# Optimization experiments

Measured on AMD Instinct MI355X. Metric: run time of the kernel, lower is better.

Reference implementation:

```python
import jax, jax.numpy as jnp
import numpy as np

N = 8192      # nodes
NIN = 128     # input feature dim
NH = 128      # hidden dim
NC = 8        # communities
CS = N // NC  # community size


def setup_inputs() -> dict:
    key = jax.random.key(0)
    k = jax.random.split(key, 6)
    seq1 = jax.random.normal(k[0], (1, N, NIN), jnp.float32)
    seq2 = jax.random.normal(k[1], (1, N, NIN), jnp.float32)
    # dense row-stochastic-ish adjacency so GCN activations stay O(1)
    adj = jax.random.uniform(k[2], (1, N, N), jnp.float32) * (2.0 / N)
    cc_label = jnp.arange(N, dtype=jnp.int32).reshape(NC, CS)  # partition of nodes
    W = jax.random.normal(k[3], (NIN, NH), jnp.float32) / np.float32(np.sqrt(NIN))
    b = jnp.zeros((NH,), jnp.float32)
    Wb = jax.random.normal(k[4], (NH, NH), jnp.float32) / np.float32(np.sqrt(NH))
    bb = jnp.zeros((), jnp.float32)
    return {"seq1": seq1, "seq2": seq2, "adj": adj, "cc_label": cc_label,
            "W": W, "b": b, "Wb": Wb, "bb": bb}


def reference(seq1, seq2, adj, cc_label, W, b, Wb, bb):
    def gcn(seq):
        fts = jnp.einsum('bnd,dh->bnh', seq, W)            # linear
        agg = jnp.einsum('bnm,bmh->bnh', adj, fts) + b     # neighborhood aggregation
        return jax.nn.relu(agg)

    h1 = gcn(seq1)[0]   # [N, NH]
    h2 = gcn(seq2)[0]   # [N, NH]

    # ragged per-community gather (communities are equal-size here)
    hg1 = h1[cc_label]  # [NC, CS, NH]
    hg2 = h2[cc_label]  # [NC, CS, NH]

    # AvgReadout (msk=None) + sigmoid -> per-community summary
    c = jax.nn.sigmoid(jnp.mean(hg1, axis=1))              # [NC, NH]

    # Discriminator: bilinear f_k(h, c) = h @ Wb @ c + bb
    cw = jnp.einsum('hk,nk->nh', Wb, c)                    # [NC, NH]
    sc1 = jnp.einsum('nch,nh->nc', hg1, cw) + bb           # [NC, CS]
    sc2 = jnp.einsum('nch,nh->nc', hg2, cw) + bb           # [NC, CS]

    # scalar scatter-back (each node written exactly once)
    flat = cc_label.reshape(-1)
    ret1 = jnp.zeros((N,), h1.dtype).at[flat].set(sc1.reshape(-1))
    ret2 = jnp.zeros((N,), h2.dtype).at[flat].set(sc2.reshape(-1))
    return jnp.concatenate([ret1, ret2])[None, :]          # [1, 2N]
```

## Files before the change

kernel.cpp:

```cpp
#include <hip/hip_runtime.h>


#define NN    8192
#define NCOLS 256
#define ASCALE 4096.0f
#define AINV  (1.0f/4096.0f)

typedef _Float16 half8 __attribute__((ext_vector_type(8)));
typedef _Float16 half4v __attribute__((ext_vector_type(4)));
typedef float    f32x4 __attribute__((ext_vector_type(4)));

__device__ __forceinline__ void gload16(const void* g, void* l) {
  __builtin_amdgcn_global_load_lds(
      (const __attribute__((address_space(1))) char*)g,
      (__attribute__((address_space(3))) char*)l, 16, 0, 0);
}

__global__ __launch_bounds__(256) void k1_fts(const float* __restrict__ seq1,
                                              const float* __restrict__ seq2,
                                              const float* __restrict__ W,
                                              _Float16* __restrict__ F,
                                              const int* __restrict__ cc,
                                              int* __restrict__ node_comm,
                                              float* __restrict__ S) {
  __shared__ char lds[65536];
  _Float16* Wt  = (_Float16*)lds;
  float*    sSeq = (float*)(lds + 32768);
  const int tid = threadIdx.x;
  const int lane = tid & 63;
  const int w = tid >> 6;
  const int l15 = lane & 15;
  const int g = lane >> 4;
  const int m0 = blockIdx.x * 64;

  if (tid < 64) {
    int i = blockIdx.x * 64 + tid;
    node_comm[cc[i]] = i >> 10;
  }
  if (blockIdx.x == 0) {
    for (int j = tid; j < 1024; j += 256) S[j] = 0.0f;
  }

  for (int it = 0; it < 64; ++it) {
    int idx = it * 256 + tid;
    int d = idx >> 7, hc = idx & 127;
    int byte = (hc * 256 + d * 2) ^ ((hc & 7) << 4);
    *(_Float16*)(lds + byte) = (_Float16)W[idx];
  }

  const float* seqp[2] = {seq1, seq2};
  const int srow = tid >> 5;
  const int sck = tid & 31;

  for (int s = 0; s < 2; ++s) {
    __syncthreads();
    const float* sp = seqp[s];
#pragma unroll
    for (int i = 0; i < 8; ++i) {
      int row = i * 8 + srow;
      gload16(sp + (size_t)(m0 + row) * 128 + ((sck ^ (row & 7)) << 2),
              (char*)sSeq + i * 4096 + w * 1024);
    }
    asm volatile("s_waitcnt vmcnt(0)" ::: "memory");
    __syncthreads();

    f32x4 acc[4][2] = {};
    const float4* S4 = (const float4*)sSeq;
    const float4* W4 = (const float4*)Wt;
#pragma unroll
    for (int kk = 0; kk < 4; ++kk) {
      half8 bf[2];
#pragma unroll
      for (int nf = 0; nf < 2; ++nf) {
        int col = w * 32 + nf * 16 + l15;
        float4 bv = W4[(col * 16 + kk * 4 + g) ^ (col & 7)];
        bf[nf] = *(const half8*)&bv;
      }
#pragma unroll
      for (int mf = 0; mf < 4; ++mf) {
        int row = mf * 16 + l15;
        int bidx = row * 32 + kk * 8 + g * 2;
        float4 u = S4[bidx ^ (row & 7)];
        float4 v = S4[(bidx + 1) ^ (row & 7)];
        half8 af;
#pragma unroll
        for (int j = 0; j < 4; ++j) af[j] = (_Float16)(((const float*)&u)[j]);
#pragma unroll
        for (int j = 0; j < 4; ++j) af[4 + j] = (_Float16)(((const float*)&v)[j]);
#pragma unroll
        for (int nf = 0; nf < 2; ++nf)
          acc[mf][nf] = __builtin_amdgcn_mfma_f32_16x16x32_f16(af, bf[nf], acc[mf][nf], 0, 0, 0);
      }
    }
    __syncthreads();
    _Float16* img = (_Float16*)sSeq;
#pragma unroll
    for (int mf = 0; mf < 4; ++mf)
#pragma unroll
      for (int nf = 0; nf < 2; ++nf) {
        int col = w * 32 + nf * 16 + l15;
#pragma unroll
        for (int j = 0; j < 4; ++j) {
          int kl = mf * 16 + g * 4 + j;
          img[(kl >> 5) * 4096 + col * 32 + (kl & 31)] = (_Float16)acc[mf][nf][j];
        }
      }
    __syncthreads();
    const float4* src4 = (const float4*)sSeq;
#pragma unroll
    for (int i = 0; i < 4; ++i) {
      int e = i * 256 + tid;
      int kt = e >> 9, off = e & 511;
      ((float4*)(F + (size_t)(2 * blockIdx.x + kt) * 8192))[s * 512 + off] = src4[e];
    }
  }
}

__global__ __launch_bounds__(512) void k2_gemm(const float* __restrict__ adj,
                                               const _Float16* __restrict__ F,
                                               float* __restrict__ Pp) {
  __shared__ __align__(16) _Float16 sA[2][32768];
  const int tid = threadIdx.x;
  const int lane = tid & 63;
  const int w = tid >> 6;
  const int l15 = lane & 15;
  const int g = lane >> 4;
  const int id = blockIdx.x;
  const int xcd = id & 7;
  const int ks = xcd >> 1;
  const int mtile = (id >> 3) * 2 + (xcd & 1);
  const int row0 = mtile * 128;
  const int wm = w >> 2, wn = w & 3;

  const float* abase = adj + (size_t)(row0 + w * 16) * NN + (size_t)ks * 2048 + lane * 4;
  const _Float16* fbase = F + (size_t)(ks * 64) * 8192;

  f32x4 acc[4][4] = {};

  auto cvt_store = [&](int b, int i, f32x4 v) {
    int row = w * 16 + i;
    char* dst = (char*)sA[b] + row * 512 + ((lane * 8) ^ ((row & 15) << 4));
    half4v h;
    h[0] = (_Float16)(v[0] * ASCALE); h[1] = (_Float16)(v[1] * ASCALE);
    h[2] = (_Float16)(v[2] * ASCALE); h[3] = (_Float16)(v[3] * ASCALE);
    *(half4v*)dst = h;
  };

  {
    f32x4 pv[16];
#pragma unroll
    for (int i = 0; i < 16; ++i)
      pv[i] = __builtin_nontemporal_load((const f32x4*)(abase + (size_t)i * NN));
#pragma unroll
    for (int i = 0; i < 16; ++i) cvt_store(0, i, pv[i]);
  }
  __syncthreads();

  int colb[4], rowb[4], rsw[4];
#pragma unroll
  for (int nf = 0; nf < 4; ++nf) colb[nf] = (wn * 64 + nf * 16 + l15) * 32 + g * 8;
#pragma unroll
  for (int mf = 0; mf < 4; ++mf) {
    int row = wm * 64 + mf * 16 + l15;
    rowb[mf] = row * 512; rsw[mf] = (row & 15) << 4;
  }

  half8 bfc[4], bfn[4];
#pragma unroll
  for (int nf = 0; nf < 4; ++nf) {
    float4 t = *(const float4*)(fbase + colb[nf]);
    bfc[nf] = *(const half8*)&t;
  }

  for (int m = 0; m < 8; ++m) {
    const int b = m & 1;
    const bool lastm = (m == 7);
    const char* ab = (const char*)sA[b];
    const float* anext = abase + (m + 1) * 256;
    f32x4 ba[8][2];
#pragma unroll
    for (int s = 0; s < 8; ++s) {
      if (!(lastm && s == 7)) {
        const _Float16* fb = fbase + (size_t)(m * 8 + s + 1) * 8192;
#pragma unroll
        for (int nf = 0; nf < 4; ++nf) {
          float4 t = *(const float4*)(fb + colb[nf]);
          bfn[nf] = *(const half8*)&t;
        }
      }
      if (!lastm) {
        ba[s][0] = __builtin_nontemporal_load((const f32x4*)(anext + (size_t)(2 * s) * NN));
        ba[s][1] = __builtin_nontemporal_load((const f32x4*)(anext + (size_t)(2 * s + 1) * NN));
      }
#pragma unroll
      for (int mf = 0; mf < 4; ++mf) {
        half8 af = *(const half8*)(ab + rowb[mf] + ((s * 64 + g * 16) ^ rsw[mf]));
#pragma unroll
        for (int nf = 0; nf < 4; ++nf)
          acc[mf][nf] = __builtin_amdgcn_mfma_f32_16x16x32_f16(af, bfc[nf], acc[mf][nf], 0, 0, 0);
      }
      if (!lastm && s >= 2) {
        cvt_store(b ^ 1, 2 * (s - 2),     ba[s - 2][0]);
        cvt_store(b ^ 1, 2 * (s - 2) + 1, ba[s - 2][1]);
      }
#pragma unroll
      for (int nf = 0; nf < 4; ++nf) bfc[nf] = bfn[nf];
    }
    if (!lastm) {
      cvt_store(b ^ 1, 12, ba[6][0]); cvt_store(b ^ 1, 13, ba[6][1]);
      cvt_store(b ^ 1, 14, ba[7][0]); cvt_store(b ^ 1, 15, ba[7][1]);
    }
    __syncthreads();
  }

#pragma unroll
  for (int mf = 0; mf < 4; ++mf)
#pragma unroll
    for (int nf = 0; nf < 4; ++nf) {
      int col = wn * 64 + nf * 16 + l15;
#pragma unroll
      for (int j = 0; j < 4; ++j) {
        int row = row0 + wm * 64 + mf * 16 + g * 4 + j;
        __builtin_nontemporal_store(acc[mf][nf][j],
            Pp + ((size_t)ks * NN + row) * NCOLS + col);
      }
    }
}

__global__ void k2r_reduce(const float* __restrict__ Pp, const float* __restrict__ b,
                           float* __restrict__ h) {
  int gid = blockIdx.x * 256 + threadIdx.x;
  size_t base = (size_t)gid * 4;
  f32x4 p0 = __builtin_nontemporal_load((const f32x4*)(Pp + base));
  f32x4 p1 = __builtin_nontemporal_load((const f32x4*)(Pp + base + 2097152));
  f32x4 p2 = __builtin_nontemporal_load((const f32x4*)(Pp + base + 4194304));
  f32x4 p3 = __builtin_nontemporal_load((const f32x4*)(Pp + base + 6291456));
  int n0 = (int)(base & 255) & 127;
  float4 r;
  r.x = fmaxf((p0[0] + p1[0] + p2[0] + p3[0]) * AINV + b[n0],     0.f);
  r.y = fmaxf((p0[1] + p1[1] + p2[1] + p3[1]) * AINV + b[n0 + 1], 0.f);
  r.z = fmaxf((p0[2] + p1[2] + p2[2] + p3[2]) * AINV + b[n0 + 2], 0.f);
  r.w = fmaxf((p0[3] + p1[3] + p2[3] + p3[3]) * AINV + b[n0 + 3], 0.f);
  *(float4*)(h + base) = r;
}

__global__ __launch_bounds__(128) void k3a_csum(const float* __restrict__ h,
                                                const int* __restrict__ node_comm,
                                                float* __restrict__ S) {
  int hh = threadIdx.x;
  int n0 = blockIdx.x * 32;
  float a0=0,a1=0,a2=0,a3=0,a4=0,a5=0,a6=0,a7=0;
  for (int i = 0; i < 32; ++i) {
    int node = n0 + i;
    int c = node_comm[node];
    float v = h[(size_t)node * 256 + hh];
    a0 += (c == 0) ? v : 0.f;  a1 += (c == 1) ? v : 0.f;
    a2 += (c == 2) ? v : 0.f;  a3 += (c == 3) ? v : 0.f;
    a4 += (c == 4) ? v : 0.f;  a5 += (c == 5) ? v : 0.f;
    a6 += (c == 6) ? v : 0.f;  a7 += (c == 7) ? v : 0.f;
  }
  if (a0 != 0.f) atomicAdd(&S[0 * 128 + hh], a0);
  if (a1 != 0.f) atomicAdd(&S[1 * 128 + hh], a1);
  if (a2 != 0.f) atomicAdd(&S[2 * 128 + hh], a2);
  if (a3 != 0.f) atomicAdd(&S[3 * 128 + hh], a3);
  if (a4 != 0.f) atomicAdd(&S[4 * 128 + hh], a4);
  if (a5 != 0.f) atomicAdd(&S[5 * 128 + hh], a5);
  if (a6 != 0.f) atomicAdd(&S[6 * 128 + hh], a6);
  if (a7 != 0.f) atomicAdd(&S[7 * 128 + hh], a7);
}

__global__ __launch_bounds__(128) void k3b_cw(const float* __restrict__ S,
                                              const float* __restrict__ Wb,
                                              float* __restrict__ cw) {
  __shared__ float sc[128];
  int ci = blockIdx.x;
  int hh = threadIdx.x;
  float m = S[ci * 128 + hh] * (1.0f / 1024.0f);
  sc[hh] = 1.0f / (1.0f + __expf(-m));
  __syncthreads();
  const float4* wr = (const float4*)(Wb + (size_t)hh * 128);
  float acc = 0.f;
#pragma unroll 8
  for (int k4 = 0; k4 < 32; ++k4) {
    float4 wv = wr[k4];
    acc += wv.x * sc[k4 * 4 + 0] + wv.y * sc[k4 * 4 + 1]
         + wv.z * sc[k4 * 4 + 2] + wv.w * sc[k4 * 4 + 3];
  }
  cw[ci * 128 + hh] = acc;
}

__global__ __launch_bounds__(256) void k5_score(const float* __restrict__ h,
                                                const int* __restrict__ node_comm,
                                                const float* __restrict__ cw,
                                                const float* __restrict__ bbp,
                                                float* __restrict__ out) {
  int tid = threadIdx.x;
  int q = tid & 15, nl = tid >> 4;
  int node = blockIdx.x * 16 + nl;
  int c = node_comm[node];
  const float* hr = h + (size_t)node * 256;
  const float* cr = cw + c * 128;
  float4 c0 = *(const float4*)(cr + q * 8);
  float4 c1 = *(const float4*)(cr + q * 8 + 4);
  float4 a0 = *(const float4*)(hr + q * 8);
  float4 a1 = *(const float4*)(hr + q * 8 + 4);
  float p1 = a0.x*c0.x + a0.y*c0.y + a0.z*c0.z + a0.w*c0.w
           + a1.x*c1.x + a1.y*c1.y + a1.z*c1.z + a1.w*c1.w;
  float4 b0 = *(const float4*)(hr + 128 + q * 8);
  float4 b1 = *(const float4*)(hr + 128 + q * 8 + 4);
  float p2 = b0.x*c0.x + b0.y*c0.y + b0.z*c0.z + b0.w*c0.w
           + b1.x*c1.x + b1.y*c1.y + b1.z*c1.z + b1.w*c1.w;
#pragma unroll
  for (int m = 8; m >= 1; m >>= 1) {
    p1 += __shfl_xor(p1, m, 64);
    p2 += __shfl_xor(p2, m, 64);
  }
  if (q == 0) {
    float bb = bbp[0];
    out[node] = p1 + bb;
    out[8192 + node] = p2 + bb;
  }
}

extern "C" void kernel_launch(void* const* d_in, const int* in_sizes, int n_in,
                              void* d_out, int out_size, void* d_ws, size_t ws_size,
                              hipStream_t stream) {
  (void)in_sizes; (void)n_in; (void)out_size; (void)ws_size;
  const float* seq1 = (const float*)d_in[0];
  const float* seq2 = (const float*)d_in[1];
  const float* adj  = (const float*)d_in[2];
  const int*   cc   = (const int*)d_in[3];
  const float* W    = (const float*)d_in[4];
  const float* b    = (const float*)d_in[5];
  const float* Wb   = (const float*)d_in[6];
  const float* bb   = (const float*)d_in[7];
  float* out = (float*)d_out;

  char* ws = (char*)d_ws;
  _Float16* F   = (_Float16*)(ws);
  float* h      = (float*)(ws + (4u << 20));
  float* Pp     = (float*)(ws + (12u << 20));
  float* S      = (float*)(ws + (44u << 20));
  float* cw     = (float*)(ws + (44u << 20) + 4096);
  int* node_comm = (int*)(ws + (44u << 20) + 8192);

  k1_fts<<<dim3(128), dim3(256), 0, stream>>>(seq1, seq2, W, F, cc, node_comm, S);
  k2_gemm<<<dim3(256), dim3(512), 0, stream>>>(adj, F, Pp);
  k2r_reduce<<<dim3(2048), dim3(256), 0, stream>>>(Pp, b, h);
  k3a_csum<<<dim3(256), dim3(128), 0, stream>>>(h, node_comm, S);
  k3b_cw<<<dim3(8), dim3(128), 0, stream>>>(S, Wb, cw);
  k5_score<<<dim3(512), dim3(256), 0, stream>>>(h, node_comm, cw, bb, out);
}
```

Measured before the change: 108.9 us.

## Fuse split-K reduce with community sums and split k1 across sequences

```diff
diff --git a/kernel.cpp b/kernel.cpp
--- a/kernel.cpp
+++ b/kernel.cpp
@@ -21,8 +21,7 @@
                                               const float* __restrict__ W,
                                               _Float16* __restrict__ F,
                                               const int* __restrict__ cc,
-                                              int* __restrict__ node_comm,
-                                              float* __restrict__ S) {
+                                              int* __restrict__ node_comm) {
   __shared__ char lds[65536];
   _Float16* Wt  = (_Float16*)lds;
   float*    sSeq = (float*)(lds + 32768);
@@ -31,88 +30,92 @@
   const int w = tid >> 6;
   const int l15 = lane & 15;
   const int g = lane >> 4;
-  const int m0 = blockIdx.x * 64;
-
-  if (tid < 64) {
-    int i = blockIdx.x * 64 + tid;
+  const int s = blockIdx.x >> 7;
+  const int mt = blockIdx.x & 127;
+  const int m0 = mt * 64;
+
+  if (s == 0 && tid < 64) {
+    int i = mt * 64 + tid;
     node_comm[cc[i]] = i >> 10;
   }
-  if (blockIdx.x == 0) {
-    for (int j = tid; j < 1024; j += 256) S[j] = 0.0f;
-  }
-
-  for (int it = 0; it < 64; ++it) {
-    int idx = it * 256 + tid;
-    int d = idx >> 7, hc = idx & 127;
-    int byte = (hc * 256 + d * 2) ^ ((hc & 7) << 4);
-    *(_Float16*)(lds + byte) = (_Float16)W[idx];
-  }
-
-  const float* seqp[2] = {seq1, seq2};
+
+  {
+    const float4* W4g = (const float4*)W;
+#pragma unroll
+    for (int i = 0; i < 16; ++i) {
+      int idx4 = i * 256 + tid;
+      float4 wv = W4g[idx4];
+      int d = idx4 >> 5;
+      int hc = (idx4 & 31) * 4;
+#pragma unroll
+      for (int j = 0; j < 4; ++j) {
+        int byte = ((hc + j) * 256 + d * 2) ^ (((hc + j) & 7) << 4);
+        *(_Float16*)(lds + byte) = (_Float16)(((const float*)&wv)[j]);
+      }
+    }
+  }
+
+  const float* sp = s ? seq2 : seq1;
   const int srow = tid >> 5;
   const int sck = tid & 31;
-
-  for (int s = 0; s < 2; ++s) {
-    __syncthreads();
-    const float* sp = seqp[s];
-#pragma unroll
-    for (int i = 0; i < 8; ++i) {
-      int row = i * 8 + srow;
-      gload16(sp + (size_t)(m0 + row) * 128 + ((sck ^ (row & 7)) << 2),
-              (char*)sSeq + i * 4096 + w * 1024);
-    }
-    asm volatile("s_waitcnt vmcnt(0)" ::: "memory");
-    __syncthreads();
-
-    f32x4 acc[4][2] = {};
-    const float4* S4 = (const float4*)sSeq;
-    const float4* W4 = (const float4*)Wt;
-#pragma unroll
-    for (int kk = 0; kk < 4; ++kk) {
-      half8 bf[2];
-#pragma unroll
-      for (int nf = 0; nf < 2; ++nf) {
-        int col = w * 32 + nf * 16 + l15;
-        float4 bv = W4[(col * 16 + kk * 4 + g) ^ (col & 7)];
-        bf[nf] = *(const half8*)&bv;
-      }
-#pragma unroll
-      for (int mf = 0; mf < 4; ++mf) {
-        int row = mf * 16 + l15;
-        int bidx = row * 32 + kk * 8 + g * 2;
-        float4 u = S4[bidx ^ (row & 7)];
-        float4 v = S4[(bidx + 1) ^ (row & 7)];
-        half8 af;
-#pragma unroll
-        for (int j = 0; j < 4; ++j) af[j] = (_Float16)(((const float*)&u)[j]);
-#pragma unroll
-        for (int j = 0; j < 4; ++j) af[4 + j] = (_Float16)(((const float*)&v)[j]);
-#pragma unroll
-        for (int nf = 0; nf < 2; ++nf)
-          acc[mf][nf] = __builtin_amdgcn_mfma_f32_16x16x32_f16(af, bf[nf], acc[mf][nf], 0, 0, 0);
-      }
-    }
-    __syncthreads();
-    _Float16* img = (_Float16*)sSeq;
-#pragma unroll
-    for (int mf = 0; mf < 4; ++mf)
-#pragma unroll
-      for (int nf = 0; nf < 2; ++nf) {
-        int col = w * 32 + nf * 16 + l15;
-#pragma unroll
-        for (int j = 0; j < 4; ++j) {
-          int kl = mf * 16 + g * 4 + j;
-          img[(kl >> 5) * 4096 + col * 32 + (kl & 31)] = (_Float16)acc[mf][nf][j];
-        }
-      }
-    __syncthreads();
-    const float4* src4 = (const float4*)sSeq;
-#pragma unroll
-    for (int i = 0; i < 4; ++i) {
-      int e = i * 256 + tid;
-      int kt = e >> 9, off = e & 511;
-      ((float4*)(F + (size_t)(2 * blockIdx.x + kt) * 8192))[s * 512 + off] = src4[e];
-    }
+  __syncthreads();
+#pragma unroll
+  for (int i = 0; i < 8; ++i) {
+    int row = i * 8 + srow;
+    gload16(sp + (size_t)(m0 + row) * 128 + ((sck ^ (row & 7)) << 2),
+            (char*)sSeq + i * 4096 + w * 1024);
+  }
+  asm volatile("s_waitcnt vmcnt(0)" ::: "memory");
+  __syncthreads();
+
+  f32x4 acc[4][2] = {};
+  const float4* S4 = (const float4*)sSeq;
+  const float4* W4 = (const float4*)Wt;
+#pragma unroll
+  for (int kk = 0; kk < 4; ++kk) {
+    half8 bf[2];
+#pragma unroll
+    for (int nf = 0; nf < 2; ++nf) {
+      int col = w * 32 + nf * 16 + l15;
+      float4 bv = W4[(col * 16 + kk * 4 + g) ^ (col & 7)];
+      bf[nf] = *(const half8*)&bv;
+    }
+#pragma unroll
+    for (int mf = 0; mf < 4; ++mf) {
+      int row = mf * 16 + l15;
+      int bidx = row * 32 + kk * 8 + g * 2;
+      float4 u = S4[bidx ^ (row & 7)];
+      float4 v = S4[(bidx + 1) ^ (row & 7)];
+      half8 af;
+#pragma unroll
+      for (int j = 0; j < 4; ++j) af[j] = (_Float16)(((const float*)&u)[j]);
+#pragma unroll
+      for (int j = 0; j < 4; ++j) af[4 + j] = (_Float16)(((const float*)&v)[j]);
+#pragma unroll
+      for (int nf = 0; nf < 2; ++nf)
+        acc[mf][nf] = __builtin_amdgcn_mfma_f32_16x16x32_f16(af, bf[nf], acc[mf][nf], 0, 0, 0);
+    }
+  }
+  __syncthreads();
+  _Float16* img = (_Float16*)sSeq;
+#pragma unroll
+  for (int mf = 0; mf < 4; ++mf)
+#pragma unroll
+    for (int nf = 0; nf < 2; ++nf) {
+      int col = w * 32 + nf * 16 + l15;
+#pragma unroll
+      for (int j = 0; j < 4; ++j) {
+        int kl = mf * 16 + g * 4 + j;
+        img[(kl >> 5) * 4096 + col * 32 + (kl & 31)] = (_Float16)acc[mf][nf][j];
+      }
+    }
+  __syncthreads();
+  const float4* src4 = (const float4*)sSeq;
+#pragma unroll
+  for (int i = 0; i < 4; ++i) {
+    int e = i * 256 + tid;
+    int kt = e >> 9, off = e & 511;
+    ((float4*)(F + (size_t)(2 * mt + kt) * 8192))[s * 512 + off] = src4[e];
   }
 }
 
@@ -227,66 +230,71 @@
     }
 }
 
-__global__ void k2r_reduce(const float* __restrict__ Pp, const float* __restrict__ b,
-                           float* __restrict__ h) {
-  int gid = blockIdx.x * 256 + threadIdx.x;
-  size_t base = (size_t)gid * 4;
-  f32x4 p0 = __builtin_nontemporal_load((const f32x4*)(Pp + base));
-  f32x4 p1 = __builtin_nontemporal_load((const f32x4*)(Pp + base + 2097152));
-  f32x4 p2 = __builtin_nontemporal_load((const f32x4*)(Pp + base + 4194304));
-  f32x4 p3 = __builtin_nontemporal_load((const f32x4*)(Pp + base + 6291456));
-  int n0 = (int)(base & 255) & 127;
-  float4 r;
-  r.x = fmaxf((p0[0] + p1[0] + p2[0] + p3[0]) * AINV + b[n0],     0.f);
-  r.y = fmaxf((p0[1] + p1[1] + p2[1] + p3[1]) * AINV + b[n0 + 1], 0.f);
-  r.z = fmaxf((p0[2] + p1[2] + p2[2] + p3[2]) * AINV + b[n0 + 2], 0.f);
-  r.w = fmaxf((p0[3] + p1[3] + p2[3] + p3[3]) * AINV + b[n0 + 3], 0.f);
-  *(float4*)(h + base) = r;
-}
-
-__global__ __launch_bounds__(128) void k3a_csum(const float* __restrict__ h,
-                                                const int* __restrict__ node_comm,
-                                                float* __restrict__ S) {
-  int hh = threadIdx.x;
-  int n0 = blockIdx.x * 32;
-  float a0=0,a1=0,a2=0,a3=0,a4=0,a5=0,a6=0,a7=0;
-  for (int i = 0; i < 32; ++i) {
-    int node = n0 + i;
-    int c = node_comm[node];
-    float v = h[(size_t)node * 256 + hh];
-    a0 += (c == 0) ? v : 0.f;  a1 += (c == 1) ? v : 0.f;
-    a2 += (c == 2) ? v : 0.f;  a3 += (c == 3) ? v : 0.f;
-    a4 += (c == 4) ? v : 0.f;  a5 += (c == 5) ? v : 0.f;
-    a6 += (c == 6) ? v : 0.f;  a7 += (c == 7) ? v : 0.f;
-  }
-  if (a0 != 0.f) atomicAdd(&S[0 * 128 + hh], a0);
-  if (a1 != 0.f) atomicAdd(&S[1 * 128 + hh], a1);
-  if (a2 != 0.f) atomicAdd(&S[2 * 128 + hh], a2);
-  if (a3 != 0.f) atomicAdd(&S[3 * 128 + hh], a3);
-  if (a4 != 0.f) atomicAdd(&S[4 * 128 + hh], a4);
-  if (a5 != 0.f) atomicAdd(&S[5 * 128 + hh], a5);
-  if (a6 != 0.f) atomicAdd(&S[6 * 128 + hh], a6);
-  if (a7 != 0.f) atomicAdd(&S[7 * 128 + hh], a7);
-}
-
-__global__ __launch_bounds__(128) void k3b_cw(const float* __restrict__ S,
-                                              const float* __restrict__ Wb,
-                                              float* __restrict__ cw) {
-  __shared__ float sc[128];
-  int ci = blockIdx.x;
-  int hh = threadIdx.x;
-  float m = S[ci * 128 + hh] * (1.0f / 1024.0f);
-  sc[hh] = 1.0f / (1.0f + __expf(-m));
-  __syncthreads();
-  const float4* wr = (const float4*)(Wb + (size_t)hh * 128);
-  float acc = 0.f;
+__global__ __launch_bounds__(256) void k2r_fused(const float* __restrict__ Pp,
+                                                 const float* __restrict__ bias,
+                                                 const int* __restrict__ node_comm,
+                                                 float* __restrict__ h,
+                                                 float* __restrict__ pB) {
+  __shared__ float sP[1024];
+  __shared__ int   sNC[32];
+  const int tid = threadIdx.x;
+  const int b = blockIdx.x;
+  if (tid < 32) sNC[tid] = node_comm[b * 32 + tid];
+  sP[tid] = 0.0f; sP[tid + 256] = 0.0f; sP[tid + 512] = 0.0f; sP[tid + 768] = 0.0f;
+  __syncthreads();
+
+  const int q = tid & 63;
+  const int r = tid >> 6;
+  const int col = q * 4;
+  const int n0 = col & 127;
+  const float b0v = bias[n0], b1v = bias[n0 + 1], b2v = bias[n0 + 2], b3v = bias[n0 + 3];
+#pragma unroll
+  for (int k = 0; k < 8; ++k) {
+    int node = b * 32 + r + 4 * k;
+    size_t idx = (size_t)node * 256 + col;
+    f32x4 p0 = __builtin_nontemporal_load((const f32x4*)(Pp + idx));
+    f32x4 p1 = __builtin_nontemporal_load((const f32x4*)(Pp + idx + 2097152));
+    f32x4 p2 = __builtin_nontemporal_load((const f32x4*)(Pp + idx + 4194304));
+    f32x4 p3 = __builtin_nontemporal_load((const f32x4*)(Pp + idx + 6291456));
+    float v0 = fmaxf((p0[0] + p1[0] + p2[0] + p3[0]) * AINV + b0v, 0.f);
+    float v1 = fmaxf((p0[1] + p1[1] + p2[1] + p3[1]) * AINV + b1v, 0.f);
+    float v2 = fmaxf((p0[2] + p1[2] + p2[2] + p3[2]) * AINV + b2v, 0.f);
+    float v3 = fmaxf((p0[3] + p1[3] + p2[3] + p3[3]) * AINV + b3v, 0.f);
+    float4 hv; hv.x = v0; hv.y = v1; hv.z = v2; hv.w = v3;
+    *(float4*)(h + idx) = hv;
+    if (col < 128) {
+      int c = sNC[r + 4 * k];
+      float* sc = &sP[c * 128 + n0];
+      atomicAdd(sc + 0, v0); atomicAdd(sc + 1, v1);
+      atomicAdd(sc + 2, v2); atomicAdd(sc + 3, v3);
+    }
+  }
+  __syncthreads();
+  float4 pv = *(const float4*)&sP[tid * 4];
+  *(float4*)(pB + (size_t)b * 1024 + tid * 4) = pv;
+}
+
+__global__ __launch_bounds__(128) void k3_cw(const float* __restrict__ pB,
+                                             const float* __restrict__ Wb,
+                                             float* __restrict__ cw) {
+  __shared__ float sig[128];
+  const int ci = blockIdx.x;
+  const int d = threadIdx.x;
+  float s = 0.f;
+#pragma unroll 8
+  for (int b = 0; b < 256; ++b)
+    s += pB[(size_t)b * 1024 + ci * 128 + d];
+  sig[d] = 1.0f / (1.0f + __expf(-s * (1.0f / 1024.0f)));
+  __syncthreads();
+  const float4* wr = (const float4*)(Wb + (size_t)d * 128);
+  const float4* s4 = (const float4*)sig;
+  float a = 0.f;
 #pragma unroll 8
   for (int k4 = 0; k4 < 32; ++k4) {
-    float4 wv = wr[k4];
-    acc += wv.x * sc[k4 * 4 + 0] + wv.y * sc[k4 * 4 + 1]
-         + wv.z * sc[k4 * 4 + 2] + wv.w * sc[k4 * 4 + 3];
-  }
-  cw[ci * 128 + hh] = acc;
+    float4 wv = wr[k4], sv = s4[k4];
+    a += wv.x * sv.x + wv.y * sv.y + wv.z * sv.z + wv.w * sv.w;
+  }
+  cw[ci * 128 + d] = a;
 }
 
 __global__ __launch_bounds__(256) void k5_score(const float* __restrict__ h,
@@ -337,17 +345,16 @@
   float* out = (float*)d_out;
 
   char* ws = (char*)d_ws;
-  _Float16* F   = (_Float16*)(ws);
-  float* h      = (float*)(ws + (4u << 20));
-  float* Pp     = (float*)(ws + (12u << 20));
-  float* S      = (float*)(ws + (44u << 20));
-  float* cw     = (float*)(ws + (44u << 20) + 4096);
-  int* node_comm = (int*)(ws + (44u << 20) + 8192);
-
-  k1_fts<<<dim3(128), dim3(256), 0, stream>>>(seq1, seq2, W, F, cc, node_comm, S);
+  _Float16* F    = (_Float16*)(ws);
+  float* h       = (float*)(ws + (4u << 20));
+  float* Pp      = (float*)(ws + (12u << 20));
+  float* pB      = (float*)(ws + (44u << 20));
+  float* cw      = (float*)(ws + (45u << 20));
+  int* node_comm = (int*)(ws + (45u << 20) + 4096);
+
+  k1_fts<<<dim3(256), dim3(256), 0, stream>>>(seq1, seq2, W, F, cc, node_comm);
   k2_gemm<<<dim3(256), dim3(512), 0, stream>>>(adj, F, Pp);
-  k2r_reduce<<<dim3(2048), dim3(256), 0, stream>>>(Pp, b, h);
-  k3a_csum<<<dim3(256), dim3(128), 0, stream>>>(h, node_comm, S);
-  k3b_cw<<<dim3(8), dim3(128), 0, stream>>>(S, Wb, cw);
+  k2r_fused<<<dim3(256), dim3(256), 0, stream>>>(Pp, b, node_comm, h, pB);
+  k3_cw<<<dim3(8), dim3(128), 0, stream>>>(pB, Wb, cw);
   k5_score<<<dim3(512), dim3(256), 0, stream>>>(h, node_comm, cw, bb, out);
 }
```

Measured after the change: 118.7 us. 9.0% more time.

## Halve split-K depth in adjacency GEMM and parallelize feature kernel over sequences

Applied to the files above, without the earlier changes.

```diff
diff --git a/kernel.cpp b/kernel.cpp
--- a/kernel.cpp
+++ b/kernel.cpp
@@ -31,95 +31,102 @@
   const int w = tid >> 6;
   const int l15 = lane & 15;
   const int g = lane >> 4;
-  const int m0 = blockIdx.x * 64;
-
-  if (tid < 64) {
-    int i = blockIdx.x * 64 + tid;
+  const int s = blockIdx.x >> 7;
+  const int mt = blockIdx.x & 127;
+  const int m0 = mt * 64;
+
+  if (s == 0 && tid < 64) {
+    int i = mt * 64 + tid;
     node_comm[cc[i]] = i >> 10;
   }
   if (blockIdx.x == 0) {
     for (int j = tid; j < 1024; j += 256) S[j] = 0.0f;
   }
 
-  for (int it = 0; it < 64; ++it) {
-    int idx = it * 256 + tid;
-    int d = idx >> 7, hc = idx & 127;
-    int byte = (hc * 256 + d * 2) ^ ((hc & 7) << 4);
-    *(_Float16*)(lds + byte) = (_Float16)W[idx];
-  }
-
-  const float* seqp[2] = {seq1, seq2};
+  {
+    const float4* W4g = (const float4*)W;
+#pragma unroll
+    for (int i = 0; i < 16; ++i) {
+      int idx4 = i * 256 + tid;
+      float4 wv = W4g[idx4];
+      int d = idx4 >> 5;
+      int hc = (idx4 & 31) * 4;
+#pragma unroll
+      for (int j = 0; j < 4; ++j) {
+        int byte = ((hc + j) * 256 + d * 2) ^ (((hc + j) & 7) << 4);
+        *(_Float16*)(lds + byte) = (_Float16)(((const float*)&wv)[j]);
+      }
+    }
+  }
+
+  const float* sp = s ? seq2 : seq1;
   const int srow = tid >> 5;
   const int sck = tid & 31;
-
-  for (int s = 0; s < 2; ++s) {
-    __syncthreads();
-    const float* sp = seqp[s];
-#pragma unroll
-    for (int i = 0; i < 8; ++i) {
-      int row = i * 8 + srow;
-      gload16(sp + (size_t)(m0 + row) * 128 + ((sck ^ (row & 7)) << 2),
-              (char*)sSeq + i * 4096 + w * 1024);
-    }
-    asm volatile("s_waitcnt vmcnt(0)" ::: "memory");
-    __syncthreads();
-
-    f32x4 acc[4][2] = {};
-    const float4* S4 = (const float4*)sSeq;
-    const float4* W4 = (const float4*)Wt;
-#pragma unroll
-    for (int kk = 0; kk < 4; ++kk) {
-      half8 bf[2];
-#pragma unroll
-      for (int nf = 0; nf < 2; ++nf) {
-        int col = w * 32 + nf * 16 + l15;
-        float4 bv = W4[(col * 16 + kk * 4 + g) ^ (col & 7)];
-        bf[nf] = *(const half8*)&bv;
-      }
-#pragma unroll
-      for (int mf = 0; mf < 4; ++mf) {
-        int row = mf * 16 + l15;
-        int bidx = row * 32 + kk * 8 + g * 2;
-        float4 u = S4[bidx ^ (row & 7)];
-        float4 v = S4[(bidx + 1) ^ (row & 7)];
-        half8 af;
-#pragma unroll
-        for (int j = 0; j < 4; ++j) af[j] = (_Float16)(((const float*)&u)[j]);
-#pragma unroll
-        for (int j = 0; j < 4; ++j) af[4 + j] = (_Float16)(((const float*)&v)[j]);
-#pragma unroll
-        for (int nf = 0; nf < 2; ++nf)
-          acc[mf][nf] = __builtin_amdgcn_mfma_f32_16x16x32_f16(af, bf[nf], acc[mf][nf], 0, 0, 0);
-      }
-    }
-    __syncthreads();
-    _Float16* img = (_Float16*)sSeq;
-#pragma unroll
-    for (int mf = 0; mf < 4; ++mf)
-#pragma unroll
-      for (int nf = 0; nf < 2; ++nf) {
-        int col = w * 32 + nf * 16 + l15;
-#pragma unroll
-        for (int j = 0; j < 4; ++j) {
-          int kl = mf * 16 + g * 4 + j;
-          img[(kl >> 5) * 4096 + col * 32 + (kl & 31)] = (_Float16)acc[mf][nf][j];
-        }
-      }
-    __syncthreads();
-    const float4* src4 = (const float4*)sSeq;
-#pragma unroll
-    for (int i = 0; i < 4; ++i) {
-      int e = i * 256 + tid;
-      int kt = e >> 9, off = e & 511;
-      ((float4*)(F + (size_t)(2 * blockIdx.x + kt) * 8192))[s * 512 + off] = src4[e];
-    }
+  __syncthreads();
+#pragma unroll
+  for (int i = 0; i < 8; ++i) {
+    int row = i * 8 + srow;
+    gload16(sp + (size_t)(m0 + row) * 128 + ((sck ^ (row & 7)) << 2),
+            (char*)sSeq + i * 4096 + w * 1024);
+  }
+  asm volatile("s_waitcnt vmcnt(0)" ::: "memory");
+  __syncthreads();
+
+  f32x4 acc[4][2] = {};
+  const float4* S4 = (const float4*)sSeq;
+  const float4* W4 = (const float4*)Wt;
+#pragma unroll
+  for (int kk = 0; kk < 4; ++kk) {
+    half8 bf[2];
+#pragma unroll
+    for (int nf = 0; nf < 2; ++nf) {
+      int col = w * 32 + nf * 16 + l15;
+      float4 bv = W4[(col * 16 + kk * 4 + g) ^ (col & 7)];
+      bf[nf] = *(const half8*)&bv;
+    }
+#pragma unroll
+    for (int mf = 0; mf < 4; ++mf) {
+      int row = mf * 16 + l15;
+      int bidx = row * 32 + kk * 8 + g * 2;
+      float4 u = S4[bidx ^ (row & 7)];
+      float4 v = S4[(bidx + 1) ^ (row & 7)];
+      half8 af;
+#pragma unroll
+      for (int j = 0; j < 4; ++j) af[j] = (_Float16)(((const float*)&u)[j]);
+#pragma unroll
+      for (int j = 0; j < 4; ++j) af[4 + j] = (_Float16)(((const float*)&v)[j]);
+#pragma unroll
+      for (int nf = 0; nf < 2; ++nf)
+        acc[mf][nf] = __builtin_amdgcn_mfma_f32_16x16x32_f16(af, bf[nf], acc[mf][nf], 0, 0, 0);
+    }
+  }
+  __syncthreads();
+  _Float16* img = (_Float16*)sSeq;
+#pragma unroll
+  for (int mf = 0; mf < 4; ++mf)
+#pragma unroll
+    for (int nf = 0; nf < 2; ++nf) {
+      int col = w * 32 + nf * 16 + l15;
+#pragma unroll
+      for (int j = 0; j < 4; ++j) {
+        int kl = mf * 16 + g * 4 + j;
+        img[(kl >> 5) * 4096 + col * 32 + (kl & 31)] = (_Float16)acc[mf][nf][j];
+      }
+    }
+  __syncthreads();
+  const float4* src4 = (const float4*)sSeq;
+#pragma unroll
+  for (int i = 0; i < 4; ++i) {
+    int e = i * 256 + tid;
+    int kt = e >> 9, off = e & 511;
+    ((float4*)(F + (size_t)(2 * mt + kt) * 8192))[s * 512 + off] = src4[e];
   }
 }
 
 __global__ __launch_bounds__(512) void k2_gemm(const float* __restrict__ adj,
                                                const _Float16* __restrict__ F,
                                                float* __restrict__ Pp) {
-  __shared__ __align__(16) _Float16 sA[2][32768];
+  __shared__ __align__(16) _Float16 sA[2][16384];
   const int tid = threadIdx.x;
   const int lane = tid & 63;
   const int w = tid >> 6;
@@ -127,18 +134,18 @@
   const int g = lane >> 4;
   const int id = blockIdx.x;
   const int xcd = id & 7;
-  const int ks = xcd >> 1;
-  const int mtile = (id >> 3) * 2 + (xcd & 1);
-  const int row0 = mtile * 128;
+  const int ks = xcd >> 2;
+  const int mtile = (id >> 3) * 4 + (xcd & 3);
+  const int row0 = mtile * 64;
   const int wm = w >> 2, wn = w & 3;
 
-  const float* abase = adj + (size_t)(row0 + w * 16) * NN + (size_t)ks * 2048 + lane * 4;
-  const _Float16* fbase = F + (size_t)(ks * 64) * 8192;
-
-  f32x4 acc[4][4] = {};
+  const float* abase = adj + (size_t)(row0 + w * 8) * NN + (size_t)ks * 4096 + lane * 4;
+  const _Float16* fbase = F + (size_t)(ks * 128) * 8192;
+
+  f32x4 acc[2][4] = {};
 
   auto cvt_store = [&](int b, int i, f32x4 v) {
-    int row = w * 16 + i;
+    int row = w * 8 + i;
     char* dst = (char*)sA[b] + row * 512 + ((lane * 8) ^ ((row & 15) << 4));
     half4v h;
     h[0] = (_Float16)(v[0] * ASCALE); h[1] = (_Float16)(v[1] * ASCALE);
@@ -147,21 +154,21 @@
   };
 
   {
-    f32x4 pv[16];
-#pragma unroll
-    for (int i = 0; i < 16; ++i)
+    f32x4 pv[8];
+#pragma unroll
+    for (int i = 0; i < 8; ++i)
       pv[i] = __builtin_nontemporal_load((const f32x4*)(abase + (size_t)i * NN));
 #pragma unroll
-    for (int i = 0; i < 16; ++i) cvt_store(0, i, pv[i]);
-  }
-  __syncthreads();
-
-  int colb[4], rowb[4], rsw[4];
+    for (int i = 0; i < 8; ++i) cvt_store(0, i, pv[i]);
+  }
+  __syncthreads();
+
+  int colb[4], rowb[2], rsw[2];
 #pragma unroll
   for (int nf = 0; nf < 4; ++nf) colb[nf] = (wn * 64 + nf * 16 + l15) * 32 + g * 8;
 #pragma unroll
-  for (int mf = 0; mf < 4; ++mf) {
-    int row = wm * 64 + mf * 16 + l15;
+  for (int mf = 0; mf < 2; ++mf) {
+    int row = wm * 32 + mf * 16 + l15;
     rowb[mf] = row * 512; rsw[mf] = (row & 15) << 4;
   }
 
@@ -172,12 +179,12 @@
     bfc[nf] = *(const half8*)&t;
   }
 
-  for (int m = 0; m < 8; ++m) {
+  for (int m = 0; m < 16; ++m) {
     const int b = m & 1;
-    const bool lastm = (m == 7);
+    const bool lastm = (m == 15);
     const char* ab = (const char*)sA[b];
     const float* anext = abase + (m + 1) * 256;
-    f32x4 ba[8][2];
+    f32x4 ba[8];
 #pragma unroll
     for (int s = 0; s < 8; ++s) {
       if (!(lastm && s == 7)) {
@@ -188,39 +195,34 @@
           bfn[nf] = *(const half8*)&t;
         }
       }
-      if (!lastm) {
-        ba[s][0] = __builtin_nontemporal_load((const f32x4*)(anext + (size_t)(2 * s) * NN));
-        ba[s][1] = __builtin_nontemporal_load((const f32x4*)(anext + (size_t)(2 * s + 1) * NN));
-      }
-#pragma unroll
-      for (int mf = 0; mf < 4; ++mf) {
+      if (!lastm)
+        ba[s] = __builtin_nontemporal_load((const f32x4*)(anext + (size_t)s * NN));
+#pragma unroll
+      for (int mf = 0; mf < 2; ++mf) {
         half8 af = *(const half8*)(ab + rowb[mf] + ((s * 64 + g * 16) ^ rsw[mf]));
 #pragma unroll
         for (int nf = 0; nf < 4; ++nf)
           acc[mf][nf] = __builtin_amdgcn_mfma_f32_16x16x32_f16(af, bfc[nf], acc[mf][nf], 0, 0, 0);
       }
-      if (!lastm && s >= 2) {
-        cvt_store(b ^ 1, 2 * (s - 2),     ba[s - 2][0]);
-        cvt_store(b ^ 1, 2 * (s - 2) + 1, ba[s - 2][1]);
-      }
+      if (!lastm && s >= 2)
+        cvt_store(b ^ 1, s - 2, ba[s - 2]);
 #pragma unroll
       for (int nf = 0; nf < 4; ++nf) bfc[nf] = bfn[nf];
     }
     if (!lastm) {
-      cvt_store(b ^ 1, 12, ba[6][0]); cvt_store(b ^ 1, 13, ba[6][1]);
-      cvt_store(b ^ 1, 14, ba[7][0]); cvt_store(b ^ 1, 15, ba[7][1]);
+      cvt_store(b ^ 1, 6, ba[6]); cvt_store(b ^ 1, 7, ba[7]);
     }
     __syncthreads();
   }
 
 #pragma unroll
-  for (int mf = 0; mf < 4; ++mf)
+  for (int mf = 0; mf < 2; ++mf)
 #pragma unroll
     for (int nf = 0; nf < 4; ++nf) {
       int col = wn * 64 + nf * 16 + l15;
 #pragma unroll
       for (int j = 0; j < 4; ++j) {
-        int row = row0 + wm * 64 + mf * 16 + g * 4 + j;
+        int row = row0 + wm * 32 + mf * 16 + g * 4 + j;
         __builtin_nontemporal_store(acc[mf][nf][j],
             Pp + ((size_t)ks * NN + row) * NCOLS + col);
       }
@@ -233,14 +235,12 @@
   size_t base = (size_t)gid * 4;
   f32x4 p0 = __builtin_nontemporal_load((const f32x4*)(Pp + base));
   f32x4 p1 = __builtin_nontemporal_load((const f32x4*)(Pp + base + 2097152));
-  f32x4 p2 = __builtin_nontemporal_load((const f32x4*)(Pp + base + 4194304));
-  f32x4 p3 = __builtin_nontemporal_load((const f32x4*)(Pp + base + 6291456));
   int n0 = (int)(base & 255) & 127;
   float4 r;
-  r.x = fmaxf((p0[0] + p1[0] + p2[0] + p3[0]) * AINV + b[n0],     0.f);
-  r.y = fmaxf((p0[1] + p1[1] + p2[1] + p3[1]) * AINV + b[n0 + 1], 0.f);
-  r.z = fmaxf((p0[2] + p1[2] + p2[2] + p3[2]) * AINV + b[n0 + 2], 0.f);
-  r.w = fmaxf((p0[3] + p1[3] + p2[3] + p3[3]) * AINV + b[n0 + 3], 0.f);
+  r.x = fmaxf((p0[0] + p1[0]) * AINV + b[n0],     0.f);
+  r.y = fmaxf((p0[1] + p1[1]) * AINV + b[n0 + 1], 0.f);
+  r.z = fmaxf((p0[2] + p1[2]) * AINV + b[n0 + 2], 0.f);
+  r.w = fmaxf((p0[3] + p1[3]) * AINV + b[n0 + 3], 0.f);
   *(float4*)(h + base) = r;
 }
 
@@ -337,14 +337,14 @@
   float* out = (float*)d_out;
 
   char* ws = (char*)d_ws;
-  _Float16* F   = (_Float16*)(ws);
-  float* h      = (float*)(ws + (4u << 20));
-  float* Pp     = (float*)(ws + (12u << 20));
-  float* S      = (float*)(ws + (44u << 20));
-  float* cw     = (float*)(ws + (44u << 20) + 4096);
+  _Float16* F    = (_Float16*)(ws);
+  float* h       = (float*)(ws + (4u << 20));
+  float* Pp      = (float*)(ws + (12u << 20));
+  float* S       = (float*)(ws + (44u << 20));
+  float* cw      = (float*)(ws + (44u << 20) + 4096);
   int* node_comm = (int*)(ws + (44u << 20) + 8192);
 
-  k1_fts<<<dim3(128), dim3(256), 0, stream>>>(seq1, seq2, W, F, cc, node_comm, S);
+  k1_fts<<<dim3(256), dim3(256), 0, stream>>>(seq1, seq2, W, F, cc, node_comm, S);
   k2_gemm<<<dim3(256), dim3(512), 0, stream>>>(adj, F, Pp);
   k2r_reduce<<<dim3(2048), dim3(256), 0, stream>>>(Pp, b, h);
   k3a_csum<<<dim3(256), dim3(128), 0, stream>>>(h, node_comm, S);
```

After: 148.6 us. 36.4% more time.
